# Kernel tuning notes

Hardware: AMD Instinct MI355X
Metric: run time of the kernel (lower is better)

The kernel has to match this reference:

```python
import jax, jax.numpy as jnp
import numpy as np

B, S, NGB, NG, DIM = 64, 4096, 13, 48, 3
NCH = [8, 8, 1]
NSHELLS = 8


def setup_inputs() -> dict:
    key = jax.random.key(0)
    ks = jax.random.split(key, 16)
    rng = np.random.default_rng(0)
    # valid row-wise permutations of the N_ngb neighbor slots per group op
    GnnPerms = jnp.asarray(np.argsort(rng.random((NG, NGB)), axis=1), dtype=jnp.int64)
    NNSites = jax.random.randint(ks[0], (NGB, S), 0, S, dtype=jnp.int64)
    SitesToShells = jax.random.randint(ks[1], (S,), 0, NSHELLS, dtype=jnp.int64)
    # block-diagonal (Ng*dim, Ng*dim) cartesian rotation blocks
    blk = rng.normal(size=(NG, DIM, DIM)).astype(np.float32) * 0.5
    gd = np.zeros((NG * DIM, NG * DIM), np.float32)
    for g in range(NG):
        gd[g * DIM:(g + 1) * DIM, g * DIM:(g + 1) * DIM] = blk[g]
    gdiags = jnp.asarray(gd)
    std = 0.2
    return {
        "InStates": jax.random.normal(ks[2], (B, 1, S), jnp.float32),
        "Psi0": jax.random.normal(ks[3], (NCH[0], 1, NGB), jnp.float32) * std,
        "bias0": jax.random.normal(ks[4], (NCH[0], 1), jnp.float32) * std,
        "Psi1": jax.random.normal(ks[5], (NCH[1], NCH[0], NGB), jnp.float32) * std,
        "bias1": jax.random.normal(ks[6], (NCH[1], 1), jnp.float32) * std,
        "Psi2": jax.random.normal(ks[7], (NCH[2], NCH[1], NGB), jnp.float32) * std,
        "bias2": jax.random.normal(ks[8], (NCH[2], 1), jnp.float32) * std,
        "wtVC": jax.random.normal(ks[9], (DIM, NGB), jnp.float32) * std,
        "ShellWeights": jax.random.normal(ks[10], (NSHELLS,), jnp.float32) * std,
        "gdiags": gdiags,
        "GnnPerms": GnnPerms,
        "NNSites": NNSites,
        "SitesToShells": SitesToShells,
    }


def _rearrange(x, NNSites):
    # x: (B, Nch, S) -> (B, Nch*N_ngb, S); subchannel j of channel c holds x[b, c, NNSites[j, s]]
    b, c, s = x.shape
    return x[:, :, NNSites].reshape(b, c * NGB, s)


def _gconv(x, W, b):
    # x: (B, NchIn*N_ngb, S); W: (NchOut, NchIn, N_ngb); b: (NchOut, 1)
    # group-rotated weights: GW[o, g, c*N_ngb+j] = W[o, c, GnnPerms[g, j]]
    GW = _gconv.GW_cache  # set per-call below via closure-free pattern; replaced in reference
    raise NotImplementedError


def reference(InStates, Psi0, bias0, Psi1, bias1, Psi2, bias2, wtVC,
              ShellWeights, gdiags, GnnPerms, NNSites, SitesToShells):
    act = jax.nn.softplus

    def gconv(x, W, b):
        # rotated weights: (NchOut, Ng, NchIn*N_ngb)
        GW = W[:, :, GnnPerms].transpose(0, 2, 1, 3).reshape(W.shape[0], NG, -1)
        h = jnp.einsum('ogk,bks->bogs', GW, x) + b[:, :, None]  # (B, NchOut, Ng, S)
        return act(h).mean(axis=2)                               # group-orbit average

    out = _rearrange(InStates, NNSites)
    for W, b in ((Psi0, bias0), (Psi1, bias1), (Psi2, bias2)):
        out = gconv(out, W, b)                 # (B, NchOut, S)
        out = _rearrange(out, NNSites)         # (B, NchOut*N_ngb, S)
    # vector channel: row g*dim+d of P is wtVC[d, GnnPerms[g]]
    P = wtVC[:, GnnPerms].transpose(1, 0, 2).reshape(NG * DIM, NGB)
    Wvc = gdiags @ P                           # (Ng*dim, N_ngb)
    v = jnp.einsum('kn,bns->bks', Wvc, out)    # (B, Ng*dim, S)
    v = v.reshape(-1, NG, DIM, out.shape[-1]).mean(axis=1)  # (B, dim, S)
    v = v * ShellWeights[SitesToShells]        # per-site shell weighting
    return v.sum(axis=2) / out.shape[-1]       # (B, dim)
```

## Files before the change

kernel.cpp:

```cpp
#include <hip/hip_runtime.h>
#include <hip/hip_bf16.h>

#define BATCH 64
#define SITES 4096
#define NGB 13
#define NGRP 48
#define SDIM 3

#define LOG2E 1.44269504f
#define SPSCALE 0.014440236f

typedef __bf16 bf16x8 __attribute__((ext_vector_type(8)));
typedef float  f32x4  __attribute__((ext_vector_type(4)));

#define OFF_AVC  0
#define OFF_U    64
#define OFF_A0   67648
#define OFF_SW   67648
#define OFF_A1   2164800
#define OFF_PART 4261952
#define UW0H 0
#define UW0L 12288
#define UW1H 24576
#define UW1L 73728
#define UW2H 122880
#define UW2L 129024

__global__ __launch_bounds__(256) void precompute_kernel(
    const float* __restrict__ Psi0, const float* __restrict__ Psi1,
    const float* __restrict__ Psi2, const float* __restrict__ wtVC,
    const float* __restrict__ gdiags, const int* __restrict__ perms,
    float* __restrict__ ws)
{
    float*  Avc = ws + OFF_AVC;
    __bf16* U   = (__bf16*)(ws + OFF_U);
    int t = blockIdx.x * 256 + threadIdx.x;
    if (t < 12288) {
        int k = t & 31, row = t >> 5;
        int o = row / NGRP, g = row - o * NGRP;
        float w = (k < NGB) ? Psi0[o * NGB + perms[g * NGB + k]] * LOG2E : 0.f;
        __bf16 hi = (__bf16)w;
        U[UW0H + t] = hi;
        U[UW0L + t] = (__bf16)(w - (float)hi);
    } else if (t < 61440) {
        int u = t - 12288;
        int k = u & 127, row = u >> 7;
        int o = row / NGRP, g = row - o * NGRP;
        float w = 0.f;
        if (k < 104) { int j = k >> 3, c = k & 7;
                       w = Psi1[(o * 8 + c) * NGB + perms[g * NGB + j]] * LOG2E; }
        __bf16 hi = (__bf16)w;
        U[UW1H + u] = hi;
        U[UW1L + u] = (__bf16)(w - (float)hi);
    } else if (t < 67584) {
        int u = t - 61440;
        int k = u & 127, g = u >> 7;
        float w = 0.f;
        if (k < 104) { int j = k >> 3, c = k & 7;
                       w = Psi2[c * NGB + perms[g * NGB + j]] * LOG2E; }
        __bf16 hi = (__bf16)w;
        U[UW2H + u] = hi;
        U[UW2L + u] = (__bf16)(w - (float)hi);
    } else if (t < 67584 + 39 * NGRP) {
        int t2 = t - 67584;
        int g = t2 % NGRP, u = t2 / NGRP;
        int d = u / NGB, n = u % NGB;
        const int row = g * SDIM + d;
        float s = 0.f;
        for (int k = 0; k < NGRP * SDIM; k++) {
            int g2 = k / SDIM, d2 = k - g2 * SDIM;
            float p = wtVC[d2 * NGB + perms[g2 * NGB + n]];
            s = fmaf(gdiags[row * (NGRP * SDIM) + k], p, s);
        }
        atomicAdd(&Avc[u], s * (1.f / 48.f));
    }
}

__global__ __launch_bounds__(256) void build_sw(
    const float* __restrict__ Avc, const int* __restrict__ NN,
    const int* __restrict__ s2sh, const float* __restrict__ shellw,
    float* __restrict__ SW)
{
    int e = blockIdx.x * 256 + threadIdx.x;
    if (e < NGB * SITES) {
        int n = e / SITES, s = e - n * SITES;
        float wgt = shellw[s2sh[s]] * (SPSCALE / (float)SITES);
        int t = NN[e];
        atomicAdd(&SW[t],             Avc[n] * wgt);
        atomicAdd(&SW[SITES + t],     Avc[NGB + n] * wgt);
        atomicAdd(&SW[2 * SITES + t], Avc[2 * NGB + n] * wgt);
    }
}

template<int NCIN, int NCTOT, int CT, int KPAD, int KSTR, int NWAVES, int NWN,
         int CHUNKS, int FUSED>
__global__ __launch_bounds__(NWAVES * 64) void layer_mfma(
    const float* __restrict__ prev,
    const __bf16* __restrict__ Wh,
    const __bf16* __restrict__ Wl,
    const float* __restrict__ bias,
    const int*   __restrict__ NN,
    const float* __restrict__ SWp,
    float* __restrict__ partial,
    float* __restrict__ out)
{
    constexpr int NTHR   = NWAVES * 64;
    constexpr int M      = NCTOT * NGRP;
    constexpr int MTILES = M / 16, NTILES = CT / 16;
    constexpr int NWM    = NWAVES / NWN;
    constexpr int MT_W   = MTILES / NWM, NT_W = NTILES / NWN;
    constexpr int KT     = KPAD / 32;
    constexpr int GS     = NGB * CT;
    constexpr int SPT    = (GS + NTHR - 1) / NTHR;
    constexpr int CPB    = SITES / CT;
    constexpr int BUF    = CT * KSTR;
    constexpr int BPB    = CPB / CHUNKS;

    static_assert(MT_W * 16 == NGRP, "wave covers exactly one o");
    static_assert(NWM * MT_W == MTILES && NWN * NT_W == NTILES, "");
    static_assert((KPAD & 31) == 0 && (KSTR & 7) == 0, "");
    static_assert(CPB % CHUNKS == 0, "block stays within one batch");

    __shared__ __bf16 xh_lds[2 * BUF];
    __shared__ __bf16 xl_lds[2 * BUF];

    const int tid  = threadIdx.x;
    const int wave = tid >> 6, lane = tid & 63;
    const int m16  = lane & 15, quad = lane >> 4;

    const int bid    = blockIdx.x;
    const int b      = bid / BPB;
    const int octet  = bid % BPB;
    const int s0base = octet * (CHUNKS * CT);

    int sj[SPT], scol[SPT];
    bool sv[SPT];
#pragma unroll
    for (int i = 0; i < SPT; i++) {
        int site = tid + i * NTHR;
        sv[i] = (site < GS);
        int ss = sv[i] ? site : 0;
        sj[i] = ss / CT;
        scol[i] = ss % CT;
    }

    auto stage_site = [&](int i, int nn, __bf16* dh, __bf16* dl) {
        if constexpr (NCIN == 1) {
            float v = prev[(size_t)b * SITES + nn];
            __bf16 hi = (__bf16)v;
            dh[scol[i] * KSTR + sj[i]] = hi;
            dl[scol[i] * KSTR + sj[i]] = (__bf16)(v - (float)hi);
        } else {
            const float4* p4 = (const float4*)(prev + ((size_t)(b * SITES + nn)) * 8);
            float4 u0 = p4[0], u1 = p4[1];
            float v[8] = {u0.x, u0.y, u0.z, u0.w, u1.x, u1.y, u1.z, u1.w};
            bf16x8 hv, lv;
#pragma unroll
            for (int c8 = 0; c8 < 8; c8++) {
                __bf16 hi = (__bf16)v[c8];
                hv[c8] = hi;
                lv[c8] = (__bf16)(v[c8] - (float)hi);
            }
            *(bf16x8*)(dh + scol[i] * KSTR + sj[i] * 8) = hv;
            *(bf16x8*)(dl + scol[i] * KSTR + sj[i] * 8) = lv;
        }
    };

    if constexpr (NCIN == 1) {
        for (int e = tid; e < 2 * CT * (KPAD - NGB); e += NTHR) {
            int buf = e / (CT * (KPAD - NGB));
            int r   = e % (CT * (KPAD - NGB));
            int col = r / (KPAD - NGB), p = r % (KPAD - NGB);
            xh_lds[buf * BUF + col * KSTR + NGB + p] = (__bf16)0.f;
            xl_lds[buf * BUF + col * KSTR + NGB + p] = (__bf16)0.f;
        }
    } else {
        const bf16x8 z8 = {};
        for (int e = tid; e < 2 * CT * 3; e += NTHR) {
            int buf = e / (CT * 3);
            int r   = e % (CT * 3);
            int col = r % CT, z = r / CT;
            *(bf16x8*)(xh_lds + buf * BUF + col * KSTR + 104 + z * 8) = z8;
            *(bf16x8*)(xl_lds + buf * BUF + col * KSTR + 104 + z * 8) = z8;
        }
    }

    int nnA[SPT];
#pragma unroll
    for (int i = 0; i < SPT; i++) if (sv[i]) {
        int nn = NN[sj[i] * SITES + s0base + scol[i]];
        stage_site(i, nn, xh_lds, xl_lds);
    }
    if (CHUNKS > 1) {
        const int s1 = s0base + CT;
#pragma unroll
        for (int i = 0; i < SPT; i++)
            nnA[i] = sv[i] ? NN[sj[i] * SITES + s1 + scol[i]] : 0;
    }
    __syncthreads();

    const int wave_mt0 = (wave / NWN) * MT_W;
    const int wave_nt0 = (wave % NWN) * NT_W;
    const int o_g      = (wave_mt0 * 16) / NGRP;
    const float bo     = bias[o_g] * LOG2E;

    float y0 = 0.f, y1 = 0.f, y2 = 0.f;

#pragma unroll 1
    for (int c = 0; c < CHUNKS; c++) {
        const int cur = c & 1;
        const __bf16* xh = xh_lds + cur * BUF;
        const __bf16* xl = xl_lds + cur * BUF;

        f32x4 acc[MT_W][NT_W];
#pragma unroll
        for (int mt = 0; mt < MT_W; mt++)
#pragma unroll
            for (int nt = 0; nt < NT_W; nt++) acc[mt][nt] = (f32x4){0.f, 0.f, 0.f, 0.f};

#pragma unroll
        for (int kt = 0; kt < KT; kt++) {
            const int koff = kt * 32 + quad * 8;
            bf16x8 ah[MT_W], al[MT_W], bh[NT_W], bl[NT_W];
#pragma unroll
            for (int mt = 0; mt < MT_W; mt++) {
                int row = (wave_mt0 + mt) * 16 + m16;
                ah[mt] = *(const bf16x8*)(Wh + (size_t)row * KPAD + koff);
                al[mt] = *(const bf16x8*)(Wl + (size_t)row * KPAD + koff);
            }
#pragma unroll
            for (int nt = 0; nt < NT_W; nt++) {
                int cbase = ((wave_nt0 + nt) * 16 + m16) * KSTR + koff;
                bh[nt] = *(const bf16x8*)(xh + cbase);
                bl[nt] = *(const bf16x8*)(xl + cbase);
            }
#pragma unroll
            for (int mt = 0; mt < MT_W; mt++)
#pragma unroll
                for (int nt = 0; nt < NT_W; nt++)
                    acc[mt][nt] = __builtin_amdgcn_mfma_f32_16x16x32_bf16(
                        ah[mt], bh[nt], acc[mt][nt], 0, 0, 0);
#pragma unroll
            for (int mt = 0; mt < MT_W; mt++)
#pragma unroll
                for (int nt = 0; nt < NT_W; nt++)
                    acc[mt][nt] = __builtin_amdgcn_mfma_f32_16x16x32_bf16(
                        al[mt], bh[nt], acc[mt][nt], 0, 0, 0);
#pragma unroll
            for (int mt = 0; mt < MT_W; mt++)
#pragma unroll
                for (int nt = 0; nt < NT_W; nt++)
                    acc[mt][nt] = __builtin_amdgcn_mfma_f32_16x16x32_bf16(
                        ah[mt], bl[nt], acc[mt][nt], 0, 0, 0);
        }

        const int s0c = s0base + c * CT;
#pragma unroll
        for (int nt = 0; nt < NT_W; nt++) {
            float s = 0.f;
#pragma unroll
            for (int mt = 0; mt < MT_W; mt++)
#pragma unroll
                for (int r = 0; r < 4; r++) {
                    float h = acc[mt][nt][r] + bo;
                    s += fmaxf(h, 0.f) + __log2f(1.f + exp2f(-fabsf(h)));
                }
            s += __shfl_xor(s, 16);
            s += __shfl_xor(s, 32);
            if (quad == 0) {
                int site = s0c + (wave_nt0 + nt) * 16 + m16;
                if constexpr (FUSED) {
                    y0 = fmaf(SWp[site],             s, y0);
                    y1 = fmaf(SWp[SITES + site],     s, y1);
                    y2 = fmaf(SWp[2 * SITES + site], s, y2);
                } else {
                    out[((size_t)(b * SITES + site)) * NCTOT + o_g] = s * SPSCALE;
                }
            }
        }

        if (c + 1 < CHUNKS) {
            __bf16* dh = xh_lds + (cur ^ 1) * BUF;
            __bf16* dl = xl_lds + (cur ^ 1) * BUF;
#pragma unroll
            for (int i = 0; i < SPT; i++) if (sv[i])
                stage_site(i, nnA[i], dh, dl);
            if (c + 2 < CHUNKS) {
                const int s2 = s0base + (c + 2) * CT;
#pragma unroll
                for (int i = 0; i < SPT; i++)
                    nnA[i] = sv[i] ? NN[sj[i] * SITES + s2 + scol[i]] : 0;
            }
        }
        __syncthreads();
    }

    if constexpr (FUSED) {
        float* red = (float*)xh_lds;
        red[tid] = y0;
        red[NTHR + tid] = y1;
        red[2 * NTHR + tid] = y2;
        __syncthreads();
        for (int st = NTHR / 2; st > 0; st >>= 1) {
            if (tid < st) {
                red[tid] += red[tid + st];
                red[NTHR + tid] += red[NTHR + tid + st];
                red[2 * NTHR + tid] += red[2 * NTHR + tid + st];
            }
            __syncthreads();
        }
        if (tid < 3) partial[bid * 3 + tid] = red[tid * NTHR];
    }
}

__global__ __launch_bounds__(256) void final_sum(
    const float* __restrict__ partial, float* __restrict__ out)
{
    int t = threadIdx.x;
    if (t < BATCH * 3) {
        int b = t / 3, d = t - b * 3;
        float s = 0.f;
        for (int o = 0; o < 8; o++) s += partial[(b * 8 + o) * 3 + d];
        out[t] = s;
    }
}

extern "C" void kernel_launch(void* const* d_in, const int* in_sizes, int n_in,
                              void* d_out, int out_size, void* d_ws, size_t ws_size,
                              hipStream_t stream)
{
    const float* InStates = (const float*)d_in[0];
    const float* Psi0     = (const float*)d_in[1];
    const float* bias0    = (const float*)d_in[2];
    const float* Psi1     = (const float*)d_in[3];
    const float* bias1    = (const float*)d_in[4];
    const float* Psi2     = (const float*)d_in[5];
    const float* bias2    = (const float*)d_in[6];
    const float* wtVC     = (const float*)d_in[7];
    const float* ShellW   = (const float*)d_in[8];
    const float* gdiags   = (const float*)d_in[9];
    const int*   GnnPerms = (const int*)d_in[10];
    const int*   NNSites  = (const int*)d_in[11];
    const int*   S2Sh     = (const int*)d_in[12];

    float*  ws   = (float*)d_ws;
    float*  Avc  = ws + OFF_AVC;
    __bf16* U    = (__bf16*)(ws + OFF_U);
    float*  A0   = ws + OFF_A0;
    float*  SW   = ws + OFF_SW;
    float*  A1   = ws + OFF_A1;
    float*  PART = ws + OFF_PART;

    float* out = (float*)d_out;

    hipMemsetAsync(Avc, 0, 64 * sizeof(float), stream);
    precompute_kernel<<<272, 256, 0, stream>>>(Psi0, Psi1, Psi2, wtVC, gdiags,
                                               GnnPerms, ws);

    constexpr int CHUNKS = 8;
    constexpr int NBLK   = BATCH * (SITES / 64) / CHUNKS;

    layer_mfma<1, 8, 64, 32, 40, 8, 1, CHUNKS, 0><<<NBLK, 512, 0, stream>>>(
        InStates, U + UW0H, U + UW0L, bias0, NNSites, nullptr, nullptr, A0);
    layer_mfma<8, 8, 64, 128, 136, 8, 1, CHUNKS, 0><<<NBLK, 512, 0, stream>>>(
        A0, U + UW1H, U + UW1L, bias1, NNSites, nullptr, nullptr, A1);

    hipMemsetAsync(SW, 0, 3 * SITES * sizeof(float), stream);
    build_sw<<<(NGB * SITES + 255) / 256, 256, 0, stream>>>(
        Avc, NNSites, S2Sh, ShellW, SW);

    layer_mfma<8, 1, 64, 128, 136, 4, 4, CHUNKS, 1><<<NBLK, 256, 0, stream>>>(
        A1, U + UW2H, U + UW2L, bias2, NNSites, SW, PART, nullptr);

    final_sum<<<1, 256, 0, stream>>>(PART, out);
}
```

Measured before the change: 310.6 us.

## Warp-specialize final layer into compute and gather-staging waves

Adds a SPLIT template mode in which half the waves run the MFMA chunk work and the other half do the neighbor gather and bf16 split staging into the next LDS buffer. Only the last fused layer uses it, launched with 8 waves instead of 4. The bias is also folded into the accumulator initialization instead of being added per element. This aims to overlap the gather latency with the matrix math, at the cost of doubling the threads per block and keeping some waves idle during each phase.

```diff
diff --git a/kernel.cpp b/kernel.cpp
--- a/kernel.cpp
+++ b/kernel.cpp
@@ -93,7 +93,7 @@
 }
 
 template<int NCIN, int NCTOT, int CT, int KPAD, int KSTR, int NWAVES, int NWN,
-         int CHUNKS, int FUSED>
+         int CHUNKS, int FUSED, int SPLIT>
 __global__ __launch_bounds__(NWAVES * 64) void layer_mfma(
     const float* __restrict__ prev,
     const __bf16* __restrict__ Wh,
@@ -105,13 +105,16 @@
     float* __restrict__ out)
 {
     constexpr int NTHR   = NWAVES * 64;
+    constexpr int NWC    = SPLIT ? NWAVES / 2 : NWAVES;
     constexpr int M      = NCTOT * NGRP;
     constexpr int MTILES = M / 16, NTILES = CT / 16;
-    constexpr int NWM    = NWAVES / NWN;
+    constexpr int NWM    = NWC / NWN;
     constexpr int MT_W   = MTILES / NWM, NT_W = NTILES / NWN;
     constexpr int KT     = KPAD / 32;
     constexpr int GS     = NGB * CT;
     constexpr int SPT    = (GS + NTHR - 1) / NTHR;
+    constexpr int PTHR   = SPLIT ? NTHR / 2 : NTHR;
+    constexpr int SPT_P  = (GS + PTHR - 1) / PTHR;
     constexpr int CPB    = SITES / CT;
     constexpr int BUF    = CT * KSTR;
     constexpr int BPB    = CPB / CHUNKS;
@@ -120,6 +123,7 @@
     static_assert(NWM * MT_W == MTILES && NWN * NT_W == NTILES, "");
     static_assert((KPAD & 31) == 0 && (KSTR & 7) == 0, "");
     static_assert(CPB % CHUNKS == 0, "block stays within one batch");
+    static_assert(!SPLIT || FUSED, "split needs linear tail");
 
     __shared__ __bf16 xh_lds[2 * BUF];
     __shared__ __bf16 xl_lds[2 * BUF];
@@ -133,23 +137,12 @@
     const int octet  = bid % BPB;
     const int s0base = octet * (CHUNKS * CT);
 
-    int sj[SPT], scol[SPT];
-    bool sv[SPT];
-#pragma unroll
-    for (int i = 0; i < SPT; i++) {
-        int site = tid + i * NTHR;
-        sv[i] = (site < GS);
-        int ss = sv[i] ? site : 0;
-        sj[i] = ss / CT;
-        scol[i] = ss % CT;
-    }
-
-    auto stage_site = [&](int i, int nn, __bf16* dh, __bf16* dl) {
+    auto stage_to = [&](int col, int j, int nn, __bf16* dh, __bf16* dl) {
         if constexpr (NCIN == 1) {
             float v = prev[(size_t)b * SITES + nn];
             __bf16 hi = (__bf16)v;
-            dh[scol[i] * KSTR + sj[i]] = hi;
-            dl[scol[i] * KSTR + sj[i]] = (__bf16)(v - (float)hi);
+            dh[col * KSTR + j] = hi;
+            dl[col * KSTR + j] = (__bf16)(v - (float)hi);
         } else {
             const float4* p4 = (const float4*)(prev + ((size_t)(b * SITES + nn)) * 8);
             float4 u0 = p4[0], u1 = p4[1];
@@ -161,8 +154,8 @@
                 hv[c8] = hi;
                 lv[c8] = (__bf16)(v[c8] - (float)hi);
             }
-            *(bf16x8*)(dh + scol[i] * KSTR + sj[i] * 8) = hv;
-            *(bf16x8*)(dl + scol[i] * KSTR + sj[i] * 8) = lv;
+            *(bf16x8*)(dh + col * KSTR + j * 8) = hv;
+            *(bf16x8*)(dl + col * KSTR + j * 8) = lv;
         }
     };
 
@@ -185,22 +178,40 @@
         }
     }
 
-    int nnA[SPT];
-#pragma unroll
-    for (int i = 0; i < SPT; i++) if (sv[i]) {
-        int nn = NN[sj[i] * SITES + s0base + scol[i]];
-        stage_site(i, nn, xh_lds, xl_lds);
-    }
-    if (CHUNKS > 1) {
-        const int s1 = s0base + CT;
-#pragma unroll
-        for (int i = 0; i < SPT; i++)
-            nnA[i] = sv[i] ? NN[sj[i] * SITES + s1 + scol[i]] : 0;
+#pragma unroll
+    for (int i = 0; i < SPT; i++) {
+        int site = tid + i * NTHR;
+        if (site < GS) {
+            int j = site / CT, col = site % CT;
+            int nn = NN[j * SITES + s0base + col];
+            stage_to(col, j, nn, xh_lds, xl_lds);
+        }
+    }
+
+    int pj[SPT_P], pcol[SPT_P], nnP[SPT_P];
+    bool pv[SPT_P];
+    {
+        const int tid2 = SPLIT ? (tid - NWC * 64) : tid;
+        const bool is_stager = SPLIT ? (wave >= NWC) : true;
+#pragma unroll
+        for (int i = 0; i < SPT_P; i++) {
+            int site = tid2 + i * PTHR;
+            pv[i] = is_stager && site >= 0 && site < GS;
+            int ss = (site >= 0 && site < GS) ? site : 0;
+            pj[i] = ss / CT;
+            pcol[i] = ss % CT;
+        }
+        if (CHUNKS > 1) {
+            const int s1 = s0base + CT;
+#pragma unroll
+            for (int i = 0; i < SPT_P; i++)
+                nnP[i] = pv[i] ? NN[pj[i] * SITES + s1 + pcol[i]] : 0;
+        }
     }
     __syncthreads();
 
-    const int wave_mt0 = (wave / NWN) * MT_W;
-    const int wave_nt0 = (wave % NWN) * NT_W;
+    const int wave_mt0 = ((wave % NWC) / NWN) * MT_W;
+    const int wave_nt0 = ((wave % NWC) % NWN) * NT_W;
     const int o_g      = (wave_mt0 * 16) / NGRP;
     const float bo     = bias[o_g] * LOG2E;
 
@@ -211,85 +222,90 @@
         const int cur = c & 1;
         const __bf16* xh = xh_lds + cur * BUF;
         const __bf16* xl = xl_lds + cur * BUF;
-
-        f32x4 acc[MT_W][NT_W];
-#pragma unroll
-        for (int mt = 0; mt < MT_W; mt++)
-#pragma unroll
-            for (int nt = 0; nt < NT_W; nt++) acc[mt][nt] = (f32x4){0.f, 0.f, 0.f, 0.f};
-
-#pragma unroll
-        for (int kt = 0; kt < KT; kt++) {
-            const int koff = kt * 32 + quad * 8;
-            bf16x8 ah[MT_W], al[MT_W], bh[NT_W], bl[NT_W];
-#pragma unroll
-            for (int mt = 0; mt < MT_W; mt++) {
-                int row = (wave_mt0 + mt) * 16 + m16;
-                ah[mt] = *(const bf16x8*)(Wh + (size_t)row * KPAD + koff);
-                al[mt] = *(const bf16x8*)(Wl + (size_t)row * KPAD + koff);
-            }
+        __bf16* dh = xh_lds + (cur ^ 1) * BUF;
+        __bf16* dl = xl_lds + (cur ^ 1) * BUF;
+
+        if (!SPLIT || wave < NWC) {
+            f32x4 acc[MT_W][NT_W];
+            const f32x4 binit = {bo, bo, bo, bo};
+#pragma unroll
+            for (int mt = 0; mt < MT_W; mt++)
+#pragma unroll
+                for (int nt = 0; nt < NT_W; nt++) acc[mt][nt] = binit;
+
+#pragma unroll
+            for (int kt = 0; kt < KT; kt++) {
+                const int koff = kt * 32 + quad * 8;
+                bf16x8 ah[MT_W], al[MT_W], bh[NT_W], bl[NT_W];
+#pragma unroll
+                for (int mt = 0; mt < MT_W; mt++) {
+                    int row = (wave_mt0 + mt) * 16 + m16;
+                    ah[mt] = *(const bf16x8*)(Wh + (size_t)row * KPAD + koff);
+                    al[mt] = *(const bf16x8*)(Wl + (size_t)row * KPAD + koff);
+                }
+#pragma unroll
+                for (int nt = 0; nt < NT_W; nt++) {
+                    int cbase = ((wave_nt0 + nt) * 16 + m16) * KSTR + koff;
+                    bh[nt] = *(const bf16x8*)(xh + cbase);
+                    bl[nt] = *(const bf16x8*)(xl + cbase);
+                }
+#pragma unroll
+                for (int mt = 0; mt < MT_W; mt++)
+#pragma unroll
+                    for (int nt = 0; nt < NT_W; nt++)
+                        acc[mt][nt] = __builtin_amdgcn_mfma_f32_16x16x32_bf16(
+                            ah[mt], bh[nt], acc[mt][nt], 0, 0, 0);
+#pragma unroll
+                for (int mt = 0; mt < MT_W; mt++)
+#pragma unroll
+                    for (int nt = 0; nt < NT_W; nt++)
+                        acc[mt][nt] = __builtin_amdgcn_mfma_f32_16x16x32_bf16(
+                            al[mt], bh[nt], acc[mt][nt], 0, 0, 0);
+#pragma unroll
+                for (int mt = 0; mt < MT_W; mt++)
+#pragma unroll
+                    for (int nt = 0; nt < NT_W; nt++)
+                        acc[mt][nt] = __builtin_amdgcn_mfma_f32_16x16x32_bf16(
+                            ah[mt], bl[nt], acc[mt][nt], 0, 0, 0);
+            }
+
+            const int s0c = s0base + c * CT;
 #pragma unroll
             for (int nt = 0; nt < NT_W; nt++) {
-                int cbase = ((wave_nt0 + nt) * 16 + m16) * KSTR + koff;
-                bh[nt] = *(const bf16x8*)(xh + cbase);
-                bl[nt] = *(const bf16x8*)(xl + cbase);
-            }
-#pragma unroll
-            for (int mt = 0; mt < MT_W; mt++)
-#pragma unroll
-                for (int nt = 0; nt < NT_W; nt++)
-                    acc[mt][nt] = __builtin_amdgcn_mfma_f32_16x16x32_bf16(
-                        ah[mt], bh[nt], acc[mt][nt], 0, 0, 0);
-#pragma unroll
-            for (int mt = 0; mt < MT_W; mt++)
-#pragma unroll
-                for (int nt = 0; nt < NT_W; nt++)
-                    acc[mt][nt] = __builtin_amdgcn_mfma_f32_16x16x32_bf16(
-                        al[mt], bh[nt], acc[mt][nt], 0, 0, 0);
-#pragma unroll
-            for (int mt = 0; mt < MT_W; mt++)
-#pragma unroll
-                for (int nt = 0; nt < NT_W; nt++)
-                    acc[mt][nt] = __builtin_amdgcn_mfma_f32_16x16x32_bf16(
-                        ah[mt], bl[nt], acc[mt][nt], 0, 0, 0);
-        }
-
-        const int s0c = s0base + c * CT;
-#pragma unroll
-        for (int nt = 0; nt < NT_W; nt++) {
-            float s = 0.f;
-#pragma unroll
-            for (int mt = 0; mt < MT_W; mt++)
-#pragma unroll
-                for (int r = 0; r < 4; r++) {
-                    float h = acc[mt][nt][r] + bo;
-                    s += fmaxf(h, 0.f) + __log2f(1.f + exp2f(-fabsf(h)));
+                float s = 0.f;
+#pragma unroll
+                for (int mt = 0; mt < MT_W; mt++)
+#pragma unroll
+                    for (int r = 0; r < 4; r++) {
+                        float h = acc[mt][nt][r];
+                        s += fmaxf(h, 0.f) + __log2f(1.f + exp2f(-fabsf(h)));
+                    }
+                s += __shfl_xor(s, 16);
+                s += __shfl_xor(s, 32);
+                if (quad == 0) {
+                    int site = s0c + (wave_nt0 + nt) * 16 + m16;
+                    if constexpr (FUSED) {
+                        y0 = fmaf(SWp[site],             s, y0);
+                        y1 = fmaf(SWp[SITES + site],     s, y1);
+                        y2 = fmaf(SWp[2 * SITES + site], s, y2);
+                    } else {
+                        out[((size_t)(b * SITES + site)) * NCTOT + o_g] = s * SPSCALE;
+                    }
                 }
-            s += __shfl_xor(s, 16);
-            s += __shfl_xor(s, 32);
-            if (quad == 0) {
-                int site = s0c + (wave_nt0 + nt) * 16 + m16;
-                if constexpr (FUSED) {
-                    y0 = fmaf(SWp[site],             s, y0);
-                    y1 = fmaf(SWp[SITES + site],     s, y1);
-                    y2 = fmaf(SWp[2 * SITES + site], s, y2);
-                } else {
-                    out[((size_t)(b * SITES + site)) * NCTOT + o_g] = s * SPSCALE;
+            }
+        }
+
+        if (c + 1 < CHUNKS) {
+            if (!SPLIT || wave >= NWC) {
+#pragma unroll
+                for (int i = 0; i < SPT_P; i++) if (pv[i])
+                    stage_to(pcol[i], pj[i], nnP[i], dh, dl);
+                if (c + 2 < CHUNKS) {
+                    const int s2 = s0base + (c + 2) * CT;
+#pragma unroll
+                    for (int i = 0; i < SPT_P; i++)
+                        nnP[i] = pv[i] ? NN[pj[i] * SITES + s2 + pcol[i]] : 0;
                 }
-            }
-        }
-
-        if (c + 1 < CHUNKS) {
-            __bf16* dh = xh_lds + (cur ^ 1) * BUF;
-            __bf16* dl = xl_lds + (cur ^ 1) * BUF;
-#pragma unroll
-            for (int i = 0; i < SPT; i++) if (sv[i])
-                stage_site(i, nnA[i], dh, dl);
-            if (c + 2 < CHUNKS) {
-                const int s2 = s0base + (c + 2) * CT;
-#pragma unroll
-                for (int i = 0; i < SPT; i++)
-                    nnA[i] = sv[i] ? NN[sj[i] * SITES + s2 + scol[i]] : 0;
             }
         }
         __syncthreads();
@@ -360,16 +376,16 @@
     constexpr int CHUNKS = 8;
     constexpr int NBLK   = BATCH * (SITES / 64) / CHUNKS;
 
-    layer_mfma<1, 8, 64, 32, 40, 8, 1, CHUNKS, 0><<<NBLK, 512, 0, stream>>>(
+    layer_mfma<1, 8, 64, 32, 40, 8, 1, CHUNKS, 0, 0><<<NBLK, 512, 0, stream>>>(
         InStates, U + UW0H, U + UW0L, bias0, NNSites, nullptr, nullptr, A0);
-    layer_mfma<8, 8, 64, 128, 136, 8, 1, CHUNKS, 0><<<NBLK, 512, 0, stream>>>(
+    layer_mfma<8, 8, 64, 128, 136, 8, 1, CHUNKS, 0, 0><<<NBLK, 512, 0, stream>>>(
         A0, U + UW1H, U + UW1L, bias1, NNSites, nullptr, nullptr, A1);
 
     hipMemsetAsync(SW, 0, 3 * SITES * sizeof(float), stream);
     build_sw<<<(NGB * SITES + 255) / 256, 256, 0, stream>>>(
         Avc, NNSites, S2Sh, ShellW, SW);
 
-    layer_mfma<8, 1, 64, 128, 136, 4, 4, CHUNKS, 1><<<NBLK, 256, 0, stream>>>(
+    layer_mfma<8, 1, 64, 128, 136, 8, 4, CHUNKS, 1, 1><<<NBLK, 512, 0, stream>>>(
         A1, U + UW2H, U + UW2L, bias2, NNSites, SW, PART, nullptr);
 
     final_sum<<<1, 256, 0, stream>>>(PART, out);
```

After: 333.5 us. +7.4%, slower.
